# Kernel tuning notes

Hardware: AMD Instinct MI355X
Metric: run time of the kernel (lower is better)

Reference implementation:

```python
import jax, jax.numpy as jnp
import numpy as np

HEADS = 8
SPLITS = 4


def setup_inputs() -> dict:
    key = jax.random.key(0)
    ks = jax.random.split(key, 5)
    B, C, N = 8, 512, 4096
    C2 = C // 2
    x = jax.random.normal(ks[0], (B, C, N), jnp.float32)
    # reduction: Conv1d(C -> C//2, k=1) => weight [C2, C], bias [C2]
    Wr = jax.random.normal(ks[1], (C2, C), jnp.float32) * (1.0 / np.sqrt(C))
    br = jnp.zeros((C2,), jnp.float32)
    # toQKV: Linear(C2 -> 3*C2, bias=False); stored as [in, out]
    Wqkv = jax.random.normal(ks[2], (C2, 3 * C2), jnp.float32) * (1.0 / np.sqrt(C2))
    # expansion: Conv1d(C2 -> C, k=1) => weight [C, C2], bias [C]
    We = jax.random.normal(ks[3], (C, C2), jnp.float32) * (1.0 / np.sqrt(C2))
    be = jnp.zeros((C,), jnp.float32)
    return {"x": x, "Wr": Wr, "br": br, "Wqkv": Wqkv, "We": We, "be": be}


def reference(x, Wr, br, Wqkv, We, be):
    B, C, N = x.shape
    h, S = HEADS, SPLITS
    # 1x1 conv reduction: [B, C, N] -> [B, C2, N]
    y = jnp.einsum('oc,bcn->bon', Wr, x) + br[None, :, None]
    t = y.transpose(0, 2, 1)                       # [B, N, C2]
    qkv = t @ Wqkv                                 # [B, N, 3*C2]
    q, k, v = jnp.split(qkv, 3, axis=-1)
    d = q.shape[-1] // h
    n = N // S

    def to_chunks(a):
        # b n (h d) -> b h S n' d  (block-diagonal chunks along the token dim)
        return a.reshape(B, N, h, d).transpose(0, 2, 1, 3).reshape(B, h, S, n, d)

    q, k, v = to_chunks(q), to_chunks(k), to_chunks(v)
    scale = d ** -0.5
    scores = jnp.einsum('bhsnd,bhsmd->bhsnm', q, k) * scale   # [B,h,S,n,n]
    attn = jax.nn.softmax(scores, axis=-1)
    o = jnp.einsum('bhsnm,bhsmd->bhsnd', attn, v)             # [B,h,S,n,d]
    # rearrange per-chunk to 'b n (h d)' and concat chunks along n (restores order)
    o = o.transpose(0, 2, 3, 1, 4).reshape(B, N, h * d)       # [B, N, C2]
    o = o.transpose(0, 2, 1)                                  # [B, C2, N]
    out = jnp.einsum('oc,bcn->bon', We, o) + be[None, :, None]  # [B, C, N]
    return out
```

## Files before the change

kernel.cpp:

```cpp
#include <hip/hip_runtime.h>
#include <hip/hip_bf16.h>

#define BATCH 8
#define CIN   512
#define NTOK  4096
#define CH    256
#define J3    768
#define NH    8
#define DH    32
#define NCH   1024

typedef _Float16 F16;
typedef _Float16 f16x8 __attribute__((ext_vector_type(8)));
typedef _Float16 f16x4 __attribute__((ext_vector_type(4)));
typedef _Float16 f16x2 __attribute__((ext_vector_type(2)));
typedef float    f32x4  __attribute__((ext_vector_type(4)));
typedef float    f32x16 __attribute__((ext_vector_type(16)));

#define QSCALE 0.25503483f


__global__ __launch_bounds__(256) void fuse_weights_kernel(
    const float* __restrict__ Wr, const float* __restrict__ br,
    const float* __restrict__ Wqkv,
    F16* __restrict__ Wc_t, float* __restrict__ bcomb)
{
    const int jb8 = blockIdx.x * 8;
    const int c = threadIdx.x;
    float acc0[8], acc1[8];
#pragma unroll
    for (int jj = 0; jj < 8; ++jj) { acc0[jj] = 0.f; acc1[jj] = 0.f; }
    for (int c2 = 0; c2 < CH; ++c2) {
        const float w0 = Wr[c2 * CIN + c];
        const float w1 = Wr[c2 * CIN + c + 256];
#pragma unroll
        for (int jj = 0; jj < 8; ++jj) {
            const float q = Wqkv[c2 * J3 + jb8 + jj];
            acc0[jj] = fmaf(w0, q, acc0[jj]);
            acc1[jj] = fmaf(w1, q, acc1[jj]);
        }
    }
    const int t0 = c >> 5, kg0 = (c >> 3) & 3, e0 = c & 7;
    const int c1 = c + 256;
    const int t1 = c1 >> 5, kg1 = (c1 >> 3) & 3, e1 = c1 & 7;
    const int jb = jb8 >> 8, row0 = jb8 & 255;
#pragma unroll
    for (int jj = 0; jj < 8; ++jj) {
        const float qs = (jb8 + jj < 256) ? QSCALE : 1.0f;
        const int row = row0 + jj;
        Wc_t[jb * 131072 + t0 * 8192 + kg0 * 2048 + row * 8 + e0] =
            (F16)(acc0[jj] * qs);
        Wc_t[jb * 131072 + t1 * 8192 + kg1 * 2048 + row * 8 + e1] =
            (F16)(acc1[jj] * qs);
    }
    if (c < 8) {
        const int j = jb8 + c;
        const float qs = (j < 256) ? QSCALE : 1.0f;
        float s = 0.f;
        for (int c2 = 0; c2 < CH; ++c2) s = fmaf(Wqkv[c2 * J3 + j], br[c2], s);
        bcomb[j] = s * qs;
    }
}

__global__ __launch_bounds__(256) void convert_we_kernel(
    const float* __restrict__ We, F16* __restrict__ We16)
{
    const int i = blockIdx.x * 256 + threadIdx.x;
    We16[i] = (F16)We[i];
}

__global__ __launch_bounds__(256) void transpose_convert_kernel(
    const float* __restrict__ x, F16* __restrict__ xt_t)
{
    const int b = blockIdx.z;
    const int c0 = blockIdx.y * 8;
    const int n = blockIdx.x * 256 + threadIdx.x;

    const float* xb = x + ((size_t)b * CIN + c0) * NTOK + n;
    f16x8 v;
#pragma unroll
    for (int i = 0; i < 8; ++i)
        v[i] = (F16)xb[(size_t)i * NTOK];

    const int nb = n >> 7, row = n & 127;
    const int t = c0 >> 5, kg = (c0 >> 3) & 3;
    *(f16x8*)&xt_t[(size_t)b * 2097152 + nb * 65536 + t * 4096 + kg * 1024 +
                   row * 8] = v;
}

__global__ __launch_bounds__(512, 4) void gemm1_kernel(
    const F16* __restrict__ A,
    const F16* __restrict__ B,
    const float* __restrict__ bias,
    F16* __restrict__ QKb,
    F16* __restrict__ Vd)
{
    const int b  = blockIdx.z;
    const int jb = blockIdx.y;
    const int j0 = jb * 256;
    const int nb = blockIdx.x;
    const int n0 = nb * 128;
    const int tid = threadIdx.x;
    const int w = tid >> 6, l = tid & 63;
    const int wr = w >> 1;
    const int wc = w & 1;
    const int cl = l & 15, rg = l >> 4;

    __shared__ __align__(16) char smem[49152];
    F16* Ash0 = (F16*)smem;
    F16* Ash1 = (F16*)(smem + 16384);
    F16* Bsh0 = (F16*)(smem + 32768);
    F16* Bsh1 = (F16*)(smem + 40960);
    F16* Esh  = (F16*)smem;

    f32x4 acc[4][4];
#pragma unroll
    for (int i = 0; i < 4; ++i)
#pragma unroll
        for (int j = 0; j < 4; ++j) acc[i][j] = (f32x4){0.f, 0.f, 0.f, 0.f};

    const F16* Abase = A + jb * 131072 + tid * 8;
    const F16* Bbase = B + (size_t)b * 2097152 + nb * 65536 + tid * 8;

#define G1_STAGE(Adst, Bdst, t)                                                \
    do {                                                                       \
        __builtin_amdgcn_global_load_lds(                                      \
            (const __attribute__((address_space(1))) void*)(Abase + (t) * 8192),\
            (__attribute__((address_space(3))) void*)&Adst[tid * 8], 16, 0, 0);\
        __builtin_amdgcn_global_load_lds(                                      \
            (const __attribute__((address_space(1))) void*)(Abase + (t) * 8192 \
                + 4096),                                                       \
            (__attribute__((address_space(3))) void*)&Adst[4096 + tid * 8],    \
            16, 0, 0);                                                         \
        __builtin_amdgcn_global_load_lds(                                      \
            (const __attribute__((address_space(1))) void*)(Bbase + (t) * 4096),\
            (__attribute__((address_space(3))) void*)&Bdst[tid * 8], 16, 0, 0);\
    } while (0)

    G1_STAGE(Ash0, Bsh0, 0);
    __syncthreads();

    for (int t = 0; t < 16; ++t) {
        F16* Ac = (t & 1) ? Ash1 : Ash0;
        F16* Bc = (t & 1) ? Bsh1 : Bsh0;
        if (t < 15) {
            F16* An = (t & 1) ? Ash0 : Ash1;
            F16* Bn = (t & 1) ? Bsh0 : Bsh1;
            G1_STAGE(An, Bn, t + 1);
        }
        f16x8 bf[4];
#pragma unroll
        for (int j = 0; j < 4; ++j)
            bf[j] = *(const f16x8*)&Bc[rg * 1024 + (wc * 64 + j * 16 + cl) * 8];
#pragma unroll
        for (int i = 0; i < 4; ++i) {
            const f16x8 af =
                *(const f16x8*)&Ac[rg * 2048 + (wr * 64 + i * 16 + cl) * 8];
#pragma unroll
            for (int j = 0; j < 4; ++j)
                acc[i][j] = __builtin_amdgcn_mfma_f32_16x16x32_f16(
                    af, bf[j], acc[i][j], 0, 0, 0);
        }
        __syncthreads();
    }
#undef G1_STAGE

    if (j0 < 512) {
        const size_t bN = (size_t)b * NTOK;
#pragma unroll
        for (int c = 0; c < 4; ++c) {
            if (c) __syncthreads();
            if (wc == (c >> 1)) {
#pragma unroll
                for (int i = 0; i < 4; ++i) {
#pragma unroll
                    for (int jj = 0; jj < 2; ++jj) {
                        const int jn = (c & 1) * 2 + jj;
                        const int nl = jj * 16 + cl;
                        const int jl = wr * 64 + i * 16 + rg * 4;
                        const int jg = j0 + jl;
                        f16x4 v;
#pragma unroll
                        for (int r = 0; r < 4; ++r)
                            v[r] = (F16)(acc[i][jn][r] + bias[jg + r]);
                        *(f16x4*)&Esh[nl * 264 + jl] = v;
                    }
                }
            }
            __syncthreads();
            const int rr = tid >> 4, ss = tid & 15;
            const f16x8 ov0 = *(const f16x8*)&Esh[rr * 264 + ss * 16];
            const f16x8 ov1 = *(const f16x8*)&Esh[rr * 264 + ss * 16 + 8];
            F16* dst = &QKb[(bN + n0 + c * 32 + rr) * 512 + j0 + ss * 16];
            *(f16x8*)dst = ov0;
            *(f16x8*)(dst + 8) = ov1;
        }
    } else {
        const size_t bD = (size_t)b * CH;
#pragma unroll
        for (int c = 0; c < 4; ++c) {
            if (c) __syncthreads();
            if (wr == c) {
#pragma unroll
                for (int i = 0; i < 4; ++i) {
                    const int jg = j0 + c * 64 + i * 16 + rg * 4;
#pragma unroll
                    for (int jn = 0; jn < 4; ++jn) {
                        const int nl = wc * 64 + jn * 16 + cl;
#pragma unroll
                        for (int r = 0; r < 4; ++r)
                            Esh[(i * 16 + rg * 4 + r) * 136 + nl] =
                                (F16)(acc[i][jn][r] + bias[jg + r]);
                    }
                }
            }
            __syncthreads();
            const int rr = tid >> 3, ss = tid & 7;
            const f16x8 ov0 = *(const f16x8*)&Esh[rr * 136 + ss * 16];
            const f16x8 ov1 = *(const f16x8*)&Esh[rr * 136 + ss * 16 + 8];
            const int dg = (j0 - 512) + c * 64 + rr;
            F16* dst = &Vd[(bD + dg) * NTOK + n0 + ss * 16];
            *(f16x8*)dst = ov0;
            *(f16x8*)(dst + 8) = ov1;
        }
    }
}

__global__ __launch_bounds__(256) void attn_mfma_kernel(
    const F16* __restrict__ QK,
    const F16* __restrict__ Vd,
    F16* __restrict__ O)
{
    const int bid = blockIdx.x;
    const int xcd = bid & 7, tt = bid >> 3;
    const int qb = tt & 7;
    const int pr = xcd * 32 + (tt >> 3);
    const int s = pr & 3, bh = pr >> 2;
    const int b = bh >> 3, h = bh & 7;
    const int tid = threadIdx.x;
    const int w = tid >> 6, l = tid & 63;
    const int ln = l & 31;
    const int hi = l >> 5;

    __shared__ __align__(16) F16 Klds[2][64 * 40];
    __shared__ __align__(16) F16 Vlds[2][32 * 68];

    const size_t bN = (size_t)b * NTOK + (size_t)s * NCH;
    const int q0 = qb * 128 + w * 32;

    const F16* Qp = QK + (bN + q0 + ln) * 512 + h * DH + hi * 8;
    const f16x8 qf0 = *(const f16x8*)Qp;
    const f16x8 qf1 = *(const f16x8*)(Qp + 16);

    const F16* Kg = QK + (bN + (tid & 63)) * 512 + 256 + h * DH + (tid >> 6) * 8;
    const F16* Vg = Vd + ((size_t)b * CH + h * DH + (tid & 31)) * NTOK
                       + (size_t)s * NCH + (tid >> 5) * 8;
    const int kw = (tid & 63) * 40 + (tid >> 6) * 8;
    const int vw = (tid & 31) * 68 + (tid >> 5) * 8;

    f16x8 kreg = *(const f16x8*)Kg;
    f16x8 vreg = *(const f16x8*)Vg;

    const f16x8 ones = {(F16)1.f, (F16)1.f, (F16)1.f, (F16)1.f,
                        (F16)1.f, (F16)1.f, (F16)1.f, (F16)1.f};

    f32x16 oacc = (f32x16)(0.0f);
    f32x16 lacc = (f32x16)(0.0f);

    *(f16x8*)&Klds[0][kw] = kreg;
    *(f16x4*)&Vlds[0][vw] = __builtin_shufflevector(vreg, vreg, 0, 1, 2, 3);
    *(f16x4*)&Vlds[0][vw + 4] = __builtin_shufflevector(vreg, vreg, 4, 5, 6, 7);

    for (int t = 0; t < 16; ++t) {
        const int cur = t & 1, nxt = cur ^ 1;
        __syncthreads();
        if (t < 15) {
            kreg = *(const f16x8*)(Kg + (size_t)(t + 1) * 64 * 512);
            vreg = *(const f16x8*)(Vg + (t + 1) * 64);
        }
        const F16* Kb = &Klds[cur][0];
        const F16* Vb = &Vlds[cur][0];
#pragma unroll
        for (int u = 0; u < 2; ++u) {
            const int nkb = u * 32;
            const f16x8 kf0 = *(const f16x8*)&Kb[(nkb + ln) * 40 + hi * 8];
            const f16x8 kf1 = *(const f16x8*)&Kb[(nkb + ln) * 40 + 16 + hi * 8];
            f32x16 sacc = (f32x16)(0.0f);
            __builtin_amdgcn_s_setprio(1);
            sacc = __builtin_amdgcn_mfma_f32_32x32x16_f16(kf0, qf0, sacc, 0, 0, 0);
            sacc = __builtin_amdgcn_mfma_f32_32x32x16_f16(kf1, qf1, sacc, 0, 0, 0);
            __builtin_amdgcn_s_setprio(0);

            union { f16x8 v; f16x2 h[4]; } pu0, pu1;
#pragma unroll
            for (int e = 0; e < 4; ++e) {
                pu0.h[e] = __builtin_bit_cast(f16x2, __builtin_amdgcn_cvt_pkrtz(
                    __builtin_amdgcn_exp2f(sacc[2 * e]),
                    __builtin_amdgcn_exp2f(sacc[2 * e + 1])));
                pu1.h[e] = __builtin_bit_cast(f16x2, __builtin_amdgcn_cvt_pkrtz(
                    __builtin_amdgcn_exp2f(sacc[8 + 2 * e]),
                    __builtin_amdgcn_exp2f(sacc[8 + 2 * e + 1])));
            }

            const int vbase = ln * 68 + nkb + 4 * hi;
            const f16x4 v00 = *(const f16x4*)&Vb[vbase];
            const f16x4 v01 = *(const f16x4*)&Vb[vbase + 8];
            const f16x4 v10 = *(const f16x4*)&Vb[vbase + 16];
            const f16x4 v11 = *(const f16x4*)&Vb[vbase + 24];
            const f16x8 vf0 = __builtin_shufflevector(v00, v01, 0, 1, 2, 3, 4, 5, 6, 7);
            const f16x8 vf1 = __builtin_shufflevector(v10, v11, 0, 1, 2, 3, 4, 5, 6, 7);

            __builtin_amdgcn_s_setprio(1);
            oacc = __builtin_amdgcn_mfma_f32_32x32x16_f16(pu0.v, vf0, oacc, 0, 0, 0);
            oacc = __builtin_amdgcn_mfma_f32_32x32x16_f16(pu1.v, vf1, oacc, 0, 0, 0);
            lacc = __builtin_amdgcn_mfma_f32_32x32x16_f16(pu0.v, ones, lacc, 0, 0, 0);
            lacc = __builtin_amdgcn_mfma_f32_32x32x16_f16(pu1.v, ones, lacc, 0, 0, 0);
            __builtin_amdgcn_s_setprio(0);
        }
        if (t < 15) {
            *(f16x8*)&Klds[nxt][kw] = kreg;
            *(f16x4*)&Vlds[nxt][vw] =
                __builtin_shufflevector(vreg, vreg, 0, 1, 2, 3);
            *(f16x4*)&Vlds[nxt][vw + 4] =
                __builtin_shufflevector(vreg, vreg, 4, 5, 6, 7);
        }
    }

    F16* Op = O + (bN + q0) * CH + h * DH + ln;
#pragma unroll
    for (int r = 0; r < 16; ++r) {
        const int qr = (r & 3) + 8 * (r >> 2) + 4 * hi;
        const float invr = __builtin_amdgcn_rcpf(lacc[r]);
        Op[(size_t)qr * CH] = (F16)(oacc[r] * invr);
    }
}

__global__ __launch_bounds__(256) void gemm2_kernel(
    const F16* __restrict__ A,
    const F16* __restrict__ B,
    const float* __restrict__ bias,
    float* __restrict__ Y)
{
    const int b  = blockIdx.z;
    const int j0 = blockIdx.y * 128;
    const int n0 = blockIdx.x * 128;
    const int tid = threadIdx.x;
    const int w = tid >> 6, l = tid & 63;
    const int wr = w >> 1, wc = w & 1;
    const int cl = l & 15, rg = l >> 4;

    __shared__ __align__(16) F16 Ash[2][4096];
    __shared__ __align__(16) F16 Bsh[2][4096];

    f32x4 acc[4][4];
#pragma unroll
    for (int i = 0; i < 4; ++i)
#pragma unroll
        for (int j = 0; j < 4; ++j) acc[i][j] = (f32x4){0.f, 0.f, 0.f, 0.f};

    const F16* Bb = B + (size_t)b * NTOK * CH;
    const int frag_off = rg * 1024 + cl * 8;

    const F16* gA0 = A  + (size_t)(j0 + l) * CH      + w * 8;
    const F16* gA1 = A  + (size_t)(j0 + 64 + l) * CH + w * 8;
    const F16* gB0 = Bb + (size_t)(n0 + l) * CH      + w * 8;
    const F16* gB1 = Bb + (size_t)(n0 + 64 + l) * CH + w * 8;

#define G2_STAGE(bu, ck)                                                       \
    do {                                                                       \
        __builtin_amdgcn_global_load_lds(                                      \
            (const __attribute__((address_space(1))) void*)(gA0 + (ck)),       \
            (__attribute__((address_space(3))) void*)&Ash[bu][w * 1024],       \
            16, 0, 0);                                                         \
        __builtin_amdgcn_global_load_lds(                                      \
            (const __attribute__((address_space(1))) void*)(gA1 + (ck)),       \
            (__attribute__((address_space(3))) void*)&Ash[bu][w * 1024 + 512], \
            16, 0, 0);                                                         \
        __builtin_amdgcn_global_load_lds(                                      \
            (const __attribute__((address_space(1))) void*)(gB0 + (ck)),       \
            (__attribute__((address_space(3))) void*)&Bsh[bu][w * 1024],       \
            16, 0, 0);                                                         \
        __builtin_amdgcn_global_load_lds(                                      \
            (const __attribute__((address_space(1))) void*)(gB1 + (ck)),       \
            (__attribute__((address_space(3))) void*)&Bsh[bu][w * 1024 + 512], \
            16, 0, 0);                                                         \
    } while (0)

    G2_STAGE(0, 0);
    __syncthreads();

    for (int t = 0; t < 8; ++t) {
        const int cur = t & 1;
        if (t < 7) G2_STAGE(cur ^ 1, (t + 1) * 32);

        f16x8 af[4], bfr[4];
#pragma unroll
        for (int f = 0; f < 4; ++f) {
            af[f]  = *(const f16x8*)&Ash[cur][frag_off + (wr * 64 + f * 16) * 8];
            bfr[f] = *(const f16x8*)&Bsh[cur][frag_off + (wc * 64 + f * 16) * 8];
        }
#pragma unroll
        for (int i = 0; i < 4; ++i)
#pragma unroll
            for (int j = 0; j < 4; ++j)
                acc[i][j] = __builtin_amdgcn_mfma_f32_16x16x32_f16(
                    af[i], bfr[j], acc[i][j], 0, 0, 0);
        __syncthreads();
    }
#undef G2_STAGE

#pragma unroll
    for (int i = 0; i < 4; ++i) {
        const int jj = j0 + wr * 64 + i * 16 + rg * 4;
#pragma unroll
        for (int j = 0; j < 4; ++j) {
            const int nn = n0 + wc * 64 + j * 16 + cl;
#pragma unroll
            for (int r = 0; r < 4; ++r)
                Y[((size_t)b * CIN + jj + r) * NTOK + nn] =
                    acc[i][j][r] + bias[jj + r];
        }
    }
}

extern "C" void kernel_launch(void* const* d_in, const int* in_sizes, int n_in,
                              void* d_out, int out_size, void* d_ws, size_t ws_size,
                              hipStream_t stream)
{
    const float* x    = (const float*)d_in[0];
    const float* Wr   = (const float*)d_in[1];
    const float* br   = (const float*)d_in[2];
    const float* Wqkv = (const float*)d_in[3];
    const float* We   = (const float*)d_in[4];
    const float* be   = (const float*)d_in[5];
    float* out = (float*)d_out;

    char* ws = (char*)d_ws;
    F16*   Wc    = (F16*)ws;      ws += 786432;
    float* bcomb = (float*)ws;    ws += 4096;
    F16*   We16  = (F16*)ws;      ws += 262144;
    F16*   QKb   = (F16*)ws;      ws += (size_t)BATCH * NTOK * 512 * 2;
    F16*   Vd    = (F16*)ws;      ws += (size_t)BATCH * CH * NTOK * 2;
    F16*   xt    = (F16*)ws;
    F16*   Obuf  = (F16*)ws;

    fuse_weights_kernel<<<J3 / 8, 256, 0, stream>>>(Wr, br, Wqkv, Wc, bcomb);
    convert_we_kernel<<<CIN * CH / 256, 256, 0, stream>>>(We, We16);
    transpose_convert_kernel<<<dim3(NTOK / 256, CIN / 8, BATCH), 256, 0, stream>>>(x, xt);
    gemm1_kernel<<<dim3(NTOK / 128, J3 / 256, BATCH), 512, 0, stream>>>(
        Wc, xt, bcomb, QKb, Vd);
    attn_mfma_kernel<<<2048, 256, 0, stream>>>(QKb, Vd, Obuf);
    gemm2_kernel<<<dim3(NTOK / 128, CIN / 128, BATCH), 256, 0, stream>>>(
        We16, Obuf, be, out);
}
```

Baseline: 188.1 us.

## Pre-tile attention output and We into gemm2 LDS layout; restructure attn inner loop

The attention epilogue now stages each wave's output tile through LDS and writes it to global memory in a tiled, chunk-contiguous layout. That layout matches what gemm2's global_load_lds expects, and We is converted into the same tiled layout, so gemm2 loads become fully contiguous 16-byte-per-thread copies instead of strided row reads. The attention inner loop is also unrolled to issue both QK^T MFMAs for the 64-key block together, interleave the oacc/lacc MFMAs, and read V fragments as single 16-byte loads with a repadded LDS stride. The cost is an extra LDS round trip and two barriers in the attention epilogue, plus more register pressure from the four live score fragments.

```diff
diff --git a/kernel.cpp b/kernel.cpp
--- a/kernel.cpp
+++ b/kernel.cpp
@@ -63,10 +63,12 @@
 }
 
 __global__ __launch_bounds__(256) void convert_we_kernel(
-    const float* __restrict__ We, F16* __restrict__ We16)
+    const float* __restrict__ We, F16* __restrict__ We_t)
 {
     const int i = blockIdx.x * 256 + threadIdx.x;
-    We16[i] = (F16)We[i];
+    const int j = i >> 8, c2 = i & 255;
+    We_t[(j >> 7) * 32768 + (c2 >> 5) * 4096 + ((c2 >> 3) & 3) * 1024 +
+         (j & 127) * 8 + (c2 & 7)] = (F16)We[i];
 }
 
 __global__ __launch_bounds__(256) void transpose_convert_kernel(
@@ -243,7 +245,7 @@
     const int hi = l >> 5;
 
     __shared__ __align__(16) F16 Klds[2][64 * 40];
-    __shared__ __align__(16) F16 Vlds[2][32 * 68];
+    __shared__ __align__(16) F16 Vlds[2][32 * 72];
 
     const size_t bN = (size_t)b * NTOK + (size_t)s * NCH;
     const int q0 = qb * 128 + w * 32;
@@ -256,7 +258,8 @@
     const F16* Vg = Vd + ((size_t)b * CH + h * DH + (tid & 31)) * NTOK
                        + (size_t)s * NCH + (tid >> 5) * 8;
     const int kw = (tid & 63) * 40 + (tid >> 6) * 8;
-    const int vw = (tid & 31) * 68 + (tid >> 5) * 8;
+    const int vg = tid >> 5;
+    const int vw = (tid & 31) * 72 + (vg >> 1) * 16 + (vg & 1) * 4;
 
     f16x8 kreg = *(const f16x8*)Kg;
     f16x8 vreg = *(const f16x8*)Vg;
@@ -269,7 +272,7 @@
 
     *(f16x8*)&Klds[0][kw] = kreg;
     *(f16x4*)&Vlds[0][vw] = __builtin_shufflevector(vreg, vreg, 0, 1, 2, 3);
-    *(f16x4*)&Vlds[0][vw + 4] = __builtin_shufflevector(vreg, vreg, 4, 5, 6, 7);
+    *(f16x4*)&Vlds[0][vw + 8] = __builtin_shufflevector(vreg, vreg, 4, 5, 6, 7);
 
     for (int t = 0; t < 16; ++t) {
         const int cur = t & 1, nxt = cur ^ 1;
@@ -280,58 +283,78 @@
         }
         const F16* Kb = &Klds[cur][0];
         const F16* Vb = &Vlds[cur][0];
-#pragma unroll
-        for (int u = 0; u < 2; ++u) {
-            const int nkb = u * 32;
-            const f16x8 kf0 = *(const f16x8*)&Kb[(nkb + ln) * 40 + hi * 8];
-            const f16x8 kf1 = *(const f16x8*)&Kb[(nkb + ln) * 40 + 16 + hi * 8];
-            f32x16 sacc = (f32x16)(0.0f);
-            __builtin_amdgcn_s_setprio(1);
-            sacc = __builtin_amdgcn_mfma_f32_32x32x16_f16(kf0, qf0, sacc, 0, 0, 0);
-            sacc = __builtin_amdgcn_mfma_f32_32x32x16_f16(kf1, qf1, sacc, 0, 0, 0);
-            __builtin_amdgcn_s_setprio(0);
-
-            union { f16x8 v; f16x2 h[4]; } pu0, pu1;
-#pragma unroll
-            for (int e = 0; e < 4; ++e) {
-                pu0.h[e] = __builtin_bit_cast(f16x2, __builtin_amdgcn_cvt_pkrtz(
-                    __builtin_amdgcn_exp2f(sacc[2 * e]),
-                    __builtin_amdgcn_exp2f(sacc[2 * e + 1])));
-                pu1.h[e] = __builtin_bit_cast(f16x2, __builtin_amdgcn_cvt_pkrtz(
-                    __builtin_amdgcn_exp2f(sacc[8 + 2 * e]),
-                    __builtin_amdgcn_exp2f(sacc[8 + 2 * e + 1])));
-            }
-
-            const int vbase = ln * 68 + nkb + 4 * hi;
-            const f16x4 v00 = *(const f16x4*)&Vb[vbase];
-            const f16x4 v01 = *(const f16x4*)&Vb[vbase + 8];
-            const f16x4 v10 = *(const f16x4*)&Vb[vbase + 16];
-            const f16x4 v11 = *(const f16x4*)&Vb[vbase + 24];
-            const f16x8 vf0 = __builtin_shufflevector(v00, v01, 0, 1, 2, 3, 4, 5, 6, 7);
-            const f16x8 vf1 = __builtin_shufflevector(v10, v11, 0, 1, 2, 3, 4, 5, 6, 7);
-
-            __builtin_amdgcn_s_setprio(1);
-            oacc = __builtin_amdgcn_mfma_f32_32x32x16_f16(pu0.v, vf0, oacc, 0, 0, 0);
-            oacc = __builtin_amdgcn_mfma_f32_32x32x16_f16(pu1.v, vf1, oacc, 0, 0, 0);
-            lacc = __builtin_amdgcn_mfma_f32_32x32x16_f16(pu0.v, ones, lacc, 0, 0, 0);
-            lacc = __builtin_amdgcn_mfma_f32_32x32x16_f16(pu1.v, ones, lacc, 0, 0, 0);
-            __builtin_amdgcn_s_setprio(0);
-        }
+
+        const f16x8 kf00 = *(const f16x8*)&Kb[ln * 40 + hi * 8];
+        const f16x8 kf01 = *(const f16x8*)&Kb[ln * 40 + 16 + hi * 8];
+        const f16x8 kf10 = *(const f16x8*)&Kb[(32 + ln) * 40 + hi * 8];
+        const f16x8 kf11 = *(const f16x8*)&Kb[(32 + ln) * 40 + 16 + hi * 8];
+        f32x16 sacc0 = (f32x16)(0.0f), sacc1 = (f32x16)(0.0f);
+        __builtin_amdgcn_s_setprio(1);
+        sacc0 = __builtin_amdgcn_mfma_f32_32x32x16_f16(kf00, qf0, sacc0, 0, 0, 0);
+        sacc1 = __builtin_amdgcn_mfma_f32_32x32x16_f16(kf10, qf0, sacc1, 0, 0, 0);
+        sacc0 = __builtin_amdgcn_mfma_f32_32x32x16_f16(kf01, qf1, sacc0, 0, 0, 0);
+        sacc1 = __builtin_amdgcn_mfma_f32_32x32x16_f16(kf11, qf1, sacc1, 0, 0, 0);
+        __builtin_amdgcn_s_setprio(0);
+
+        union { f16x8 v; f16x2 h[4]; } pu00, pu01, pu10, pu11;
+#pragma unroll
+        for (int e = 0; e < 4; ++e) {
+            pu00.h[e] = __builtin_bit_cast(f16x2, __builtin_amdgcn_cvt_pkrtz(
+                __builtin_amdgcn_exp2f(sacc0[2 * e]),
+                __builtin_amdgcn_exp2f(sacc0[2 * e + 1])));
+            pu01.h[e] = __builtin_bit_cast(f16x2, __builtin_amdgcn_cvt_pkrtz(
+                __builtin_amdgcn_exp2f(sacc0[8 + 2 * e]),
+                __builtin_amdgcn_exp2f(sacc0[8 + 2 * e + 1])));
+            pu10.h[e] = __builtin_bit_cast(f16x2, __builtin_amdgcn_cvt_pkrtz(
+                __builtin_amdgcn_exp2f(sacc1[2 * e]),
+                __builtin_amdgcn_exp2f(sacc1[2 * e + 1])));
+            pu11.h[e] = __builtin_bit_cast(f16x2, __builtin_amdgcn_cvt_pkrtz(
+                __builtin_amdgcn_exp2f(sacc1[8 + 2 * e]),
+                __builtin_amdgcn_exp2f(sacc1[8 + 2 * e + 1])));
+        }
+
+        const int vb = ln * 72 + hi * 8;
+        const f16x8 vf00 = *(const f16x8*)&Vb[vb];
+        const f16x8 vf01 = *(const f16x8*)&Vb[vb + 16];
+        const f16x8 vf10 = *(const f16x8*)&Vb[vb + 32];
+        const f16x8 vf11 = *(const f16x8*)&Vb[vb + 48];
+
+        __builtin_amdgcn_s_setprio(1);
+        oacc = __builtin_amdgcn_mfma_f32_32x32x16_f16(pu00.v, vf00, oacc, 0, 0, 0);
+        lacc = __builtin_amdgcn_mfma_f32_32x32x16_f16(pu00.v, ones, lacc, 0, 0, 0);
+        oacc = __builtin_amdgcn_mfma_f32_32x32x16_f16(pu01.v, vf01, oacc, 0, 0, 0);
+        lacc = __builtin_amdgcn_mfma_f32_32x32x16_f16(pu01.v, ones, lacc, 0, 0, 0);
+        oacc = __builtin_amdgcn_mfma_f32_32x32x16_f16(pu10.v, vf10, oacc, 0, 0, 0);
+        lacc = __builtin_amdgcn_mfma_f32_32x32x16_f16(pu10.v, ones, lacc, 0, 0, 0);
+        oacc = __builtin_amdgcn_mfma_f32_32x32x16_f16(pu11.v, vf11, oacc, 0, 0, 0);
+        lacc = __builtin_amdgcn_mfma_f32_32x32x16_f16(pu11.v, ones, lacc, 0, 0, 0);
+        __builtin_amdgcn_s_setprio(0);
+
         if (t < 15) {
             *(f16x8*)&Klds[nxt][kw] = kreg;
             *(f16x4*)&Vlds[nxt][vw] =
                 __builtin_shufflevector(vreg, vreg, 0, 1, 2, 3);
-            *(f16x4*)&Vlds[nxt][vw + 4] =
+            *(f16x4*)&Vlds[nxt][vw + 8] =
                 __builtin_shufflevector(vreg, vreg, 4, 5, 6, 7);
         }
     }
 
-    F16* Op = O + (bN + q0) * CH + h * DH + ln;
+    __syncthreads();
+    F16* Elds = (F16*)&Klds[0][0] + w * 1152;
 #pragma unroll
     for (int r = 0; r < 16; ++r) {
         const int qr = (r & 3) + 8 * (r >> 2) + 4 * hi;
         const float invr = __builtin_amdgcn_rcpf(lacc[r]);
-        Op[(size_t)qr * CH] = (F16)(oacc[r] * invr);
+        Elds[qr * 36 + ln] = (F16)(oacc[r] * invr);
+    }
+    __syncthreads();
+    F16* Ob = O + (size_t)b * 1048576 + (s * 8 + qb) * 32768 + h * 4096;
+    const int q = l & 31;
+#pragma unroll
+    for (int st = 0; st < 2; ++st) {
+        const int kg = (l >> 5) + 2 * st;
+        const f16x8 ov = *(const f16x8*)&Elds[q * 36 + kg * 8];
+        *(f16x8*)&Ob[kg * 1024 + (w * 32 + q) * 8] = ov;
     }
 }
 
@@ -342,8 +365,10 @@
     float* __restrict__ Y)
 {
     const int b  = blockIdx.z;
-    const int j0 = blockIdx.y * 128;
-    const int n0 = blockIdx.x * 128;
+    const int jb = blockIdx.y;
+    const int j0 = jb * 128;
+    const int nb = blockIdx.x;
+    const int n0 = nb * 128;
     const int tid = threadIdx.x;
     const int w = tid >> 6, l = tid & 63;
     const int wr = w >> 1, wc = w & 1;
@@ -358,31 +383,29 @@
 #pragma unroll
         for (int j = 0; j < 4; ++j) acc[i][j] = (f32x4){0.f, 0.f, 0.f, 0.f};
 
-    const F16* Bb = B + (size_t)b * NTOK * CH;
     const int frag_off = rg * 1024 + cl * 8;
-
-    const F16* gA0 = A  + (size_t)(j0 + l) * CH      + w * 8;
-    const F16* gA1 = A  + (size_t)(j0 + 64 + l) * CH + w * 8;
-    const F16* gB0 = Bb + (size_t)(n0 + l) * CH      + w * 8;
-    const F16* gB1 = Bb + (size_t)(n0 + 64 + l) * CH + w * 8;
-
-#define G2_STAGE(bu, ck)                                                       \
+    const F16* Abase = A + jb * 32768 + tid * 8;
+    const F16* Bbase = B + (size_t)b * 1048576 + nb * 32768 + tid * 8;
+
+#define G2_STAGE(bu, t)                                                        \
     do {                                                                       \
         __builtin_amdgcn_global_load_lds(                                      \
-            (const __attribute__((address_space(1))) void*)(gA0 + (ck)),       \
-            (__attribute__((address_space(3))) void*)&Ash[bu][w * 1024],       \
+            (const __attribute__((address_space(1))) void*)(Abase + (t) * 4096),\
+            (__attribute__((address_space(3))) void*)&Ash[bu][tid * 8],        \
             16, 0, 0);                                                         \
         __builtin_amdgcn_global_load_lds(                                      \
-            (const __attribute__((address_space(1))) void*)(gA1 + (ck)),       \
-            (__attribute__((address_space(3))) void*)&Ash[bu][w * 1024 + 512], \
+            (const __attribute__((address_space(1))) void*)(Abase + (t) * 4096 \
+                + 2048),                                                       \
+            (__attribute__((address_space(3))) void*)&Ash[bu][2048 + tid * 8], \
             16, 0, 0);                                                         \
         __builtin_amdgcn_global_load_lds(                                      \
-            (const __attribute__((address_space(1))) void*)(gB0 + (ck)),       \
-            (__attribute__((address_space(3))) void*)&Bsh[bu][w * 1024],       \
+            (const __attribute__((address_space(1))) void*)(Bbase + (t) * 4096),\
+            (__attribute__((address_space(3))) void*)&Bsh[bu][tid * 8],        \
             16, 0, 0);                                                         \
         __builtin_amdgcn_global_load_lds(                                      \
-            (const __attribute__((address_space(1))) void*)(gB1 + (ck)),       \
-            (__attribute__((address_space(3))) void*)&Bsh[bu][w * 1024 + 512], \
+            (const __attribute__((address_space(1))) void*)(Bbase + (t) * 4096 \
+                + 2048),                                                       \
+            (__attribute__((address_space(3))) void*)&Bsh[bu][2048 + tid * 8], \
             16, 0, 0);                                                         \
     } while (0)
 
@@ -391,7 +414,7 @@
 
     for (int t = 0; t < 8; ++t) {
         const int cur = t & 1;
-        if (t < 7) G2_STAGE(cur ^ 1, (t + 1) * 32);
+        if (t < 7) G2_STAGE(cur ^ 1, t + 1);
 
         f16x8 af[4], bfr[4];
 #pragma unroll
@@ -438,18 +461,18 @@
     char* ws = (char*)d_ws;
     F16*   Wc    = (F16*)ws;      ws += 786432;
     float* bcomb = (float*)ws;    ws += 4096;
-    F16*   We16  = (F16*)ws;      ws += 262144;
+    F16*   We_t  = (F16*)ws;      ws += 262144;
     F16*   QKb   = (F16*)ws;      ws += (size_t)BATCH * NTOK * 512 * 2;
     F16*   Vd    = (F16*)ws;      ws += (size_t)BATCH * CH * NTOK * 2;
     F16*   xt    = (F16*)ws;
-    F16*   Obuf  = (F16*)ws;
+    F16*   O_t   = (F16*)ws;
 
     fuse_weights_kernel<<<J3 / 8, 256, 0, stream>>>(Wr, br, Wqkv, Wc, bcomb);
-    convert_we_kernel<<<CIN * CH / 256, 256, 0, stream>>>(We, We16);
+    convert_we_kernel<<<CIN * CH / 256, 256, 0, stream>>>(We, We_t);
     transpose_convert_kernel<<<dim3(NTOK / 256, CIN / 8, BATCH), 256, 0, stream>>>(x, xt);
     gemm1_kernel<<<dim3(NTOK / 128, J3 / 256, BATCH), 512, 0, stream>>>(
         Wc, xt, bcomb, QKb, Vd);
-    attn_mfma_kernel<<<2048, 256, 0, stream>>>(QKb, Vd, Obuf);
+    attn_mfma_kernel<<<2048, 256, 0, stream>>>(QKb, Vd, O_t);
     gemm2_kernel<<<dim3(NTOK / 128, CIN / 128, BATCH), 256, 0, stream>>>(
-        We16, Obuf, be, out);
-}
+        We_t, O_t, be, out);
+}
```

Result: no change. 186.8 us (-0.7%).

## Pre-tile We and attention output so gemm2 stages contiguous LDS blocks

Applied to the files above, without the earlier changes.

Stores the expansion weights and the attention output in a pre-tiled fragment layout (per 128-row block, per 32-channel k-slice). The attention epilogue now stages its results through LDS so each wave writes 16-byte vectors, replacing scattered 2-byte stores. gemm2 then loads each stage as a contiguous 8 KB block per operand instead of strided rows. This adds an extra LDS round trip and two barriers in the attention epilogue, and it ties the buffer layouts of the producer and consumer kernels to each other.

```diff
diff --git a/kernel.cpp b/kernel.cpp
--- a/kernel.cpp
+++ b/kernel.cpp
@@ -63,10 +63,12 @@
 }
 
 __global__ __launch_bounds__(256) void convert_we_kernel(
-    const float* __restrict__ We, F16* __restrict__ We16)
+    const float* __restrict__ We, F16* __restrict__ We_t)
 {
     const int i = blockIdx.x * 256 + threadIdx.x;
-    We16[i] = (F16)We[i];
+    const int j = i >> 8, c2 = i & 255;
+    We_t[(j >> 7) * 32768 + (c2 >> 5) * 4096 + ((c2 >> 3) & 3) * 1024 +
+         (j & 127) * 8 + (c2 & 7)] = (F16)We[i];
 }
 
 __global__ __launch_bounds__(256) void transpose_convert_kernel(
@@ -326,12 +328,22 @@
         }
     }
 
-    F16* Op = O + (bN + q0) * CH + h * DH + ln;
+    __syncthreads();
+    F16* Elds = (F16*)&Klds[0][0] + w * 1152;
 #pragma unroll
     for (int r = 0; r < 16; ++r) {
         const int qr = (r & 3) + 8 * (r >> 2) + 4 * hi;
         const float invr = __builtin_amdgcn_rcpf(lacc[r]);
-        Op[(size_t)qr * CH] = (F16)(oacc[r] * invr);
+        Elds[qr * 36 + ln] = (F16)(oacc[r] * invr);
+    }
+    __syncthreads();
+    F16* Ob = O + (size_t)b * 1048576 + (s * 8 + qb) * 32768 + h * 4096;
+    const int q = l & 31;
+#pragma unroll
+    for (int st = 0; st < 2; ++st) {
+        const int kg = (l >> 5) + 2 * st;
+        const f16x8 ov = *(const f16x8*)&Elds[q * 36 + kg * 8];
+        *(f16x8*)&Ob[kg * 1024 + (w * 32 + q) * 8] = ov;
     }
 }
 
@@ -342,8 +354,10 @@
     float* __restrict__ Y)
 {
     const int b  = blockIdx.z;
-    const int j0 = blockIdx.y * 128;
-    const int n0 = blockIdx.x * 128;
+    const int jb = blockIdx.y;
+    const int j0 = jb * 128;
+    const int nb = blockIdx.x;
+    const int n0 = nb * 128;
     const int tid = threadIdx.x;
     const int w = tid >> 6, l = tid & 63;
     const int wr = w >> 1, wc = w & 1;
@@ -358,31 +372,29 @@
 #pragma unroll
         for (int j = 0; j < 4; ++j) acc[i][j] = (f32x4){0.f, 0.f, 0.f, 0.f};
 
-    const F16* Bb = B + (size_t)b * NTOK * CH;
     const int frag_off = rg * 1024 + cl * 8;
-
-    const F16* gA0 = A  + (size_t)(j0 + l) * CH      + w * 8;
-    const F16* gA1 = A  + (size_t)(j0 + 64 + l) * CH + w * 8;
-    const F16* gB0 = Bb + (size_t)(n0 + l) * CH      + w * 8;
-    const F16* gB1 = Bb + (size_t)(n0 + 64 + l) * CH + w * 8;
-
-#define G2_STAGE(bu, ck)                                                       \
+    const F16* Abase = A + jb * 32768 + tid * 8;
+    const F16* Bbase = B + (size_t)b * 1048576 + nb * 32768 + tid * 8;
+
+#define G2_STAGE(bu, t)                                                        \
     do {                                                                       \
         __builtin_amdgcn_global_load_lds(                                      \
-            (const __attribute__((address_space(1))) void*)(gA0 + (ck)),       \
-            (__attribute__((address_space(3))) void*)&Ash[bu][w * 1024],       \
+            (const __attribute__((address_space(1))) void*)(Abase + (t) * 4096),\
+            (__attribute__((address_space(3))) void*)&Ash[bu][tid * 8],        \
             16, 0, 0);                                                         \
         __builtin_amdgcn_global_load_lds(                                      \
-            (const __attribute__((address_space(1))) void*)(gA1 + (ck)),       \
-            (__attribute__((address_space(3))) void*)&Ash[bu][w * 1024 + 512], \
+            (const __attribute__((address_space(1))) void*)(Abase + (t) * 4096 \
+                + 2048),                                                       \
+            (__attribute__((address_space(3))) void*)&Ash[bu][2048 + tid * 8], \
             16, 0, 0);                                                         \
         __builtin_amdgcn_global_load_lds(                                      \
-            (const __attribute__((address_space(1))) void*)(gB0 + (ck)),       \
-            (__attribute__((address_space(3))) void*)&Bsh[bu][w * 1024],       \
+            (const __attribute__((address_space(1))) void*)(Bbase + (t) * 4096),\
+            (__attribute__((address_space(3))) void*)&Bsh[bu][tid * 8],        \
             16, 0, 0);                                                         \
         __builtin_amdgcn_global_load_lds(                                      \
-            (const __attribute__((address_space(1))) void*)(gB1 + (ck)),       \
-            (__attribute__((address_space(3))) void*)&Bsh[bu][w * 1024 + 512], \
+            (const __attribute__((address_space(1))) void*)(Bbase + (t) * 4096 \
+                + 2048),                                                       \
+            (__attribute__((address_space(3))) void*)&Bsh[bu][2048 + tid * 8], \
             16, 0, 0);                                                         \
     } while (0)
 
@@ -391,7 +403,7 @@
 
     for (int t = 0; t < 8; ++t) {
         const int cur = t & 1;
-        if (t < 7) G2_STAGE(cur ^ 1, (t + 1) * 32);
+        if (t < 7) G2_STAGE(cur ^ 1, t + 1);
 
         f16x8 af[4], bfr[4];
 #pragma unroll
@@ -438,18 +450,18 @@
     char* ws = (char*)d_ws;
     F16*   Wc    = (F16*)ws;      ws += 786432;
     float* bcomb = (float*)ws;    ws += 4096;
-    F16*   We16  = (F16*)ws;      ws += 262144;
+    F16*   We_t  = (F16*)ws;      ws += 262144;
     F16*   QKb   = (F16*)ws;      ws += (size_t)BATCH * NTOK * 512 * 2;
     F16*   Vd    = (F16*)ws;      ws += (size_t)BATCH * CH * NTOK * 2;
     F16*   xt    = (F16*)ws;
-    F16*   Obuf  = (F16*)ws;
+    F16*   O_t   = (F16*)ws;
 
     fuse_weights_kernel<<<J3 / 8, 256, 0, stream>>>(Wr, br, Wqkv, Wc, bcomb);
-    convert_we_kernel<<<CIN * CH / 256, 256, 0, stream>>>(We, We16);
+    convert_we_kernel<<<CIN * CH / 256, 256, 0, stream>>>(We, We_t);
     transpose_convert_kernel<<<dim3(NTOK / 256, CIN / 8, BATCH), 256, 0, stream>>>(x, xt);
     gemm1_kernel<<<dim3(NTOK / 128, J3 / 256, BATCH), 512, 0, stream>>>(
         Wc, xt, bcomb, QKb, Vd);
-    attn_mfma_kernel<<<2048, 256, 0, stream>>>(QKb, Vd, Obuf);
+    attn_mfma_kernel<<<2048, 256, 0, stream>>>(QKb, Vd, O_t);
     gemm2_kernel<<<dim3(NTOK / 128, CIN / 128, BATCH), 256, 0, stream>>>(
-        We16, Obuf, be, out);
-}
+        We_t, O_t, be, out);
+}
```

Measured after the change: 181.9 us. -3.3%, faster.
